# Kernel tuning notes

Hardware: AMD Instinct MI355X
Metric: run time of the kernel (lower is better)

## Reference

```python
import jax, jax.numpy as jnp
import numpy as np

DIM = 1024
HEADS = 16
HEAD_DIM = DIM // HEADS

def setup_inputs() -> dict:
    key = jax.random.key(0)
    ks = jax.random.split(key, 6)
    s = 0.02
    return {
        "x": jax.random.normal(ks[0], (2, 2048, DIM), dtype=jnp.float32),
        "w_qkv": jax.random.normal(ks[1], (DIM, 3 * DIM), dtype=jnp.float32) * s,
        "w_proj": jax.random.normal(ks[2], (DIM, DIM), dtype=jnp.float32) * s,
        "b_proj": jnp.zeros((DIM,), dtype=jnp.float32),
        "ln_gamma": jnp.ones((DIM,), dtype=jnp.float32),
        "ln_beta": jnp.zeros((DIM,), dtype=jnp.float32),
    }

def layer_norm(x, gamma, beta, eps=1e-5):
    mu = jnp.mean(x, axis=-1, keepdims=True)
    var = jnp.var(x, axis=-1, keepdims=True)
    return (x - mu) * jax.lax.rsqrt(var + eps) * gamma + beta

def reference(x, w_qkv, w_proj, b_proj, ln_gamma, ln_beta):
    B, N, C = x.shape
    residual = x
    h = layer_norm(x, ln_gamma, ln_beta)
    qkv = h @ w_qkv  # [B,N,3C]
    qkv = qkv.reshape(B, N, 3, HEADS, HEAD_DIM)
    q = jnp.transpose(qkv[:, :, 0], (0, 2, 1, 3))  # [B,H,N,D]
    k = jnp.transpose(qkv[:, :, 1], (0, 2, 1, 3))
    v = jnp.transpose(qkv[:, :, 2], (0, 2, 1, 3))
    scale = 1.0 / jnp.sqrt(jnp.float32(HEAD_DIM))
    attn = jnp.einsum('bhqd,bhkd->bhqk', q, k) * scale
    attn = jax.nn.softmax(attn, axis=-1)
    out = jnp.einsum('bhqk,bhkd->bhqd', attn, v)  # [B,H,N,D]
    out = jnp.transpose(out, (0, 2, 1, 3)).reshape(B, N, C)
    out = out @ w_proj + b_proj
    return out + residual
```

## Files before the change

kernel.cpp:

```cpp
#include <hip/hip_runtime.h>

#define DIM   1024
#define HEADS 16
#define HDIM  64
#define BATCH 2
#define SEQ   2048
#define TOK   (BATCH*SEQ)
#define MEG   1048576

typedef __bf16 bf16x8 __attribute__((ext_vector_type(8)));
typedef float  f32x4  __attribute__((ext_vector_type(4)));

__device__ __forceinline__ float b2f(ushort u) {
    union { unsigned int u32; float f; } x; x.u32 = ((unsigned int)u) << 16; return x.f;
}
__device__ __forceinline__ ushort f2b(float f) {
    union { float f; unsigned int u32; } x; x.f = f;
    unsigned int r = x.u32 + 0x7FFFu + ((x.u32 >> 16) & 1u);
    return (ushort)(r >> 16);
}
__device__ __forceinline__ unsigned int pack2bf(float a, float b) {
    union { float f; unsigned int u; } xa, xb; xa.f = a; xb.f = b;
    return (xb.u & 0xFFFF0000u) | (xa.u >> 16);
}
__device__ __forceinline__ void gload_lds16(const ushort* g, void* l) {
    __builtin_amdgcn_global_load_lds((const __attribute__((address_space(1))) void*)g,
                                     (__attribute__((address_space(3))) void*)l, 16, 0, 0);
}

__global__ void transpose_f2b_k(const float* __restrict__ src, ushort* __restrict__ dst,
                                int R, int Cc) {
    __shared__ ushort tile[32][33];
    int c0 = blockIdx.x * 32, r0 = blockIdx.y * 32;
    int tx = threadIdx.x, ty = threadIdx.y;
#pragma unroll
    for (int i = 0; i < 4; i++)
        tile[ty + 8 * i][tx] = f2b(src[(long)(r0 + ty + 8 * i) * Cc + c0 + tx]);
    __syncthreads();
#pragma unroll
    for (int i = 0; i < 4; i++)
        dst[(long)(c0 + ty + 8 * i) * R + r0 + tx] = tile[tx][ty + 8 * i];
}

__global__ __launch_bounds__(256)
void ln_k(const float* __restrict__ x, const float* __restrict__ gamma,
          const float* __restrict__ beta, ushort* __restrict__ h) {
    __shared__ float red[8];
    int row = blockIdx.x, tid = threadIdx.x;
    const float* xr = x + (long)row * DIM;
    float4 xv = *(const float4*)(xr + tid * 4);
    float s1 = xv.x + xv.y + xv.z + xv.w;
    float s2 = xv.x * xv.x + xv.y * xv.y + xv.z * xv.z + xv.w * xv.w;
#pragma unroll
    for (int off = 32; off; off >>= 1) {
        s1 += __shfl_down(s1, off);
        s2 += __shfl_down(s2, off);
    }
    int wid = tid >> 6, lane = tid & 63;
    if (lane == 0) { red[wid * 2] = s1; red[wid * 2 + 1] = s2; }
    __syncthreads();
    s1 = red[0] + red[2] + red[4] + red[6];
    s2 = red[1] + red[3] + red[5] + red[7];
    float mu  = s1 * (1.0f / DIM);
    float var = s2 * (1.0f / DIM) - mu * mu;
    float rs  = rsqrtf(var + 1e-5f);
    float4 gv = *(const float4*)(gamma + tid * 4);
    float4 bv = *(const float4*)(beta + tid * 4);
    ushort4 ov;
    ov.x = f2b((xv.x - mu) * rs * gv.x + bv.x);
    ov.y = f2b((xv.y - mu) * rs * gv.y + bv.y);
    ov.z = f2b((xv.z - mu) * rs * gv.z + bv.z);
    ov.w = f2b((xv.w - mu) * rs * gv.w + bv.w);
    *(ushort4*)(h + (long)row * DIM + tid * 4) = ov;
}

__global__ __launch_bounds__(256, 3)
void gemm_qkv_k(const ushort* __restrict__ A, const ushort* __restrict__ Bt,
                ushort* __restrict__ qp, ushort* __restrict__ kp, ushort* __restrict__ vp) {
    __shared__ ushort smem[16384];
    int tid  = threadIdx.x;
    int wid  = tid >> 6, lane = tid & 63;
    int quad = lane >> 4, l16 = lane & 15;
    int wm = wid >> 1, wn = wid & 1;
    int rowbase = blockIdx.y * 128;
    int colbase = blockIdx.x * 128;

    f32x4 acc[4][4];
#pragma unroll
    for (int i = 0; i < 4; i++)
#pragma unroll
        for (int j = 0; j < 4; j++) acc[i][j] = (f32x4){0.f, 0.f, 0.f, 0.f};

    for (int k0 = 0; k0 < DIM; k0 += 64) {
#pragma unroll
        for (int p = 0; p < 2; p++) {
            int c = wid * 2 + p;
            int r = c * 16 + (lane >> 2);
            int ac = (lane & 3) * 8;
#pragma unroll
            for (int pnl = 0; pnl < 2; pnl++) {
                int cc = k0 + pnl * 32 + ac;
                gload_lds16(A  + (long)(rowbase + r) * DIM + cc,
                            &smem[pnl * 4096 + c * 16 * 32]);
                gload_lds16(Bt + (long)(colbase + r) * DIM + cc,
                            &smem[8192 + pnl * 4096 + c * 16 * 32]);
            }
        }
        __syncthreads();
#pragma unroll
        for (int pnl = 0; pnl < 2; pnl++) {
            bf16x8 fa[4], fb[4];
#pragma unroll
            for (int t = 0; t < 4; t++)
                fa[t] = *(const bf16x8*)(&smem[pnl * 4096 + (wm * 64 + t * 16 + l16) * 32 + quad * 8]);
#pragma unroll
            for (int t = 0; t < 4; t++)
                fb[t] = *(const bf16x8*)(&smem[8192 + pnl * 4096 + (wn * 64 + t * 16 + l16) * 32 + quad * 8]);
#pragma unroll
            for (int i = 0; i < 4; i++)
#pragma unroll
                for (int j = 0; j < 4; j++)
                    acc[i][j] = __builtin_amdgcn_mfma_f32_16x16x32_bf16(fa[i], fb[j], acc[i][j], 0, 0, 0);
        }
        __syncthreads();
    }

    if (colbase >= 2048) {
#pragma unroll
        for (int i = 0; i < 4; i++)
#pragma unroll
            for (int j = 0; j < 4; j++) {
                int cl = wn * 64 + j * 16 + l16;
                int rl = wm * 64 + i * 16 + quad * 4;
#pragma unroll
                for (int r = 0; r < 4; r++)
                    smem[cl * 128 + rl + r] = f2b(acc[i][j][r]);
            }
        __syncthreads();
        int b = rowbase >> 11, nnb = rowbase & 2047;
        int hbase = (colbase - 2048) >> 6;
#pragma unroll
        for (int i = 0; i < 8; i++) {
            int id = i * 256 + tid;
            int cl = id >> 4;
            int off = (id & 15) * 8;
            int hh = hbase + (cl >> 6), d = cl & 63;
            uint4 val = *(const uint4*)(&smem[cl * 128 + off]);
            *(uint4*)(vp + (((long)b * HEADS + hh) * HDIM + d) * SEQ + nnb + off) = val;
        }
    } else {
#pragma unroll
        for (int i = 0; i < 4; i++)
#pragma unroll
            for (int j = 0; j < 4; j++) {
                int m0  = rowbase + wm * 64 + i * 16 + quad * 4;
                int col = colbase + wn * 64 + j * 16 + l16;
                int part = col >> 10, rem = col & 1023;
                int head = rem >> 6, d = rem & 63;
                ushort* dst = (part == 0) ? qp : kp;
#pragma unroll
                for (int r = 0; r < 4; r++) {
                    float v = acc[i][j][r];
                    int mm = m0 + r;
                    int b = mm >> 11, nn = mm & 2047;
                    float sv = (part == 0) ? v * 0.125f : v;
                    dst[((((long)b * HEADS + head) * SEQ + nn) << 6) + d] = f2b(sv);
                }
            }
    }
}

__global__ __launch_bounds__(256, 3)
void gemm_proj_k(const ushort* __restrict__ A, const ushort* __restrict__ Bt,
                 const float* __restrict__ bias, const float* __restrict__ xres,
                 float* __restrict__ outp) {
    __shared__ ushort As[2][128][32];
    __shared__ ushort Bs[2][64][32];
    int tid  = threadIdx.x;
    int wid  = tid >> 6, lane = tid & 63;
    int quad = lane >> 4, l16 = lane & 15;
    int rowbase = blockIdx.y * 128;
    int colbase = blockIdx.x * 64;
    int arow = lane >> 2, acol = (lane & 3) * 8;

    f32x4 acc[2][4];
#pragma unroll
    for (int i = 0; i < 2; i++)
#pragma unroll
        for (int j = 0; j < 4; j++) acc[i][j] = (f32x4){0.f, 0.f, 0.f, 0.f};

    for (int k0 = 0; k0 < DIM; k0 += 64) {
#pragma unroll
        for (int p = 0; p < 2; p++) {
            int c = wid * 2 + p;
            int r = c * 16 + arow;
            int mm = rowbase + r;
            int bq = mm >> 11, nn = mm & 2047;
#pragma unroll
            for (int pnl = 0; pnl < 2; pnl++) {
                int cc = k0 + pnl * 32 + acol;
                int head = cc >> 6, d = cc & 63;
                gload_lds16(A + ((((long)bq * HEADS + head) * SEQ + nn) << 6) + d,
                            &As[pnl][c * 16][0]);
            }
        }
        {
            int r = wid * 16 + arow;
#pragma unroll
            for (int pnl = 0; pnl < 2; pnl++) {
                int cc = k0 + pnl * 32 + acol;
                gload_lds16(Bt + (long)(colbase + r) * DIM + cc, &Bs[pnl][wid * 16][0]);
            }
        }
        __syncthreads();
#pragma unroll
        for (int pnl = 0; pnl < 2; pnl++) {
            bf16x8 fa[2], fb[4];
#pragma unroll
            for (int t = 0; t < 2; t++)
                fa[t] = *(const bf16x8*)(&As[pnl][wid * 32 + t * 16 + l16][quad * 8]);
#pragma unroll
            for (int t = 0; t < 4; t++)
                fb[t] = *(const bf16x8*)(&Bs[pnl][t * 16 + l16][quad * 8]);
#pragma unroll
            for (int i = 0; i < 2; i++)
#pragma unroll
                for (int j = 0; j < 4; j++)
                    acc[i][j] = __builtin_amdgcn_mfma_f32_16x16x32_bf16(fa[i], fb[j], acc[i][j], 0, 0, 0);
        }
        __syncthreads();
    }

#pragma unroll
    for (int i = 0; i < 2; i++)
#pragma unroll
        for (int j = 0; j < 4; j++) {
            int m0  = rowbase + wid * 32 + i * 16 + quad * 4;
            int col = colbase + j * 16 + l16;
#pragma unroll
            for (int r = 0; r < 4; r++) {
                int mm = m0 + r;
                outp[(long)mm * DIM + col] = acc[i][j][r] + bias[col] + xres[(long)mm * DIM + col];
            }
        }
}

__global__ __launch_bounds__(256, 2)
void attn_k(ushort* qio, const ushort* __restrict__ k,
            const ushort* __restrict__ vt) {
    __shared__ ushort Kp[2][2][2304];
    __shared__ ushort Vs[2][4608];
    __shared__ ushort plds[4][2][1152];
    int bh = blockIdx.y;
    int tid = threadIdx.x, wid = tid >> 6, lane = tid & 63;
    int quad = lane >> 4, l16 = lane & 15;
    ushort* qh = qio + (long)bh * SEQ * HDIM;
    const ushort* kh = k  + (long)bh * SEQ * HDIM;
    const ushort* vh = vt + (long)bh * HDIM * SEQ;

    int krow = tid & 31, kc8 = (tid >> 5) * 8;
    int kpan = kc8 >> 5, kcp = kc8 & 31;
    int koff = krow * 72 + kcp;
    int vrow = tid & 63, vcol = (tid >> 6) * 8;
    int voff = vrow * 72 + vcol;

    int qrow0 = blockIdx.x * 128 + wid * 32;
    bf16x8 qf[2][2];
#pragma unroll
    for (int s = 0; s < 2; s++) {
        qf[s][0] = *(const bf16x8*)(qh + (long)(qrow0 + s * 16 + l16) * HDIM + quad * 8);
        qf[s][1] = *(const bf16x8*)(qh + (long)(qrow0 + s * 16 + l16) * HDIM + 32 + quad * 8);
    }

    f32x4 o[2][4];
    f32x4 lac[2][2];
#pragma unroll
    for (int s = 0; s < 2; s++) {
#pragma unroll
        for (int dc = 0; dc < 4; dc++) o[s][dc] = (f32x4){0.f, 0.f, 0.f, 0.f};
        lac[s][0] = (f32x4){0.f, 0.f, 0.f, 0.f};
        lac[s][1] = (f32x4){0.f, 0.f, 0.f, 0.f};
    }

    uint4 kreg = *(const uint4*)(kh + (long)krow * HDIM + kc8);
    uint4 vreg = *(const uint4*)(vh + (long)vrow * SEQ + vcol);
    *(uint4*)(&Kp[0][kpan][koff]) = kreg;
    *(uint4*)(&Vs[0][voff]) = vreg;

    const int NIT = SEQ / 32;
    for (int it = 0; it < NIT; ++it) {
        int buf = it & 1;
        if (it + 1 < NIT) {
            int kt = (it + 1) * 32;
            kreg = *(const uint4*)(kh + (long)(kt + krow) * HDIM + kc8);
            vreg = *(const uint4*)(vh + (long)vrow * SEQ + kt + vcol);
        }
        __syncthreads();

        bf16x8 kb[2][2];
#pragma unroll
        for (int t = 0; t < 2; t++)
#pragma unroll
            for (int p = 0; p < 2; p++)
                kb[t][p] = *(const bf16x8*)(&Kp[buf][p][(t * 16 + l16) * 72 + quad * 8]);

        f32x4 sc[2][2];
#pragma unroll
        for (int s = 0; s < 2; s++)
#pragma unroll
            for (int t = 0; t < 2; t++) {
                f32x4 z = (f32x4){0.f, 0.f, 0.f, 0.f};
                z = __builtin_amdgcn_mfma_f32_16x16x32_bf16(kb[t][0], qf[s][0], z, 0, 0, 0);
                z = __builtin_amdgcn_mfma_f32_16x16x32_bf16(kb[t][1], qf[s][1], z, 0, 0, 0);
                sc[s][t] = z;
            }

#pragma unroll
        for (int s = 0; s < 2; s++)
#pragma unroll
            for (int t = 0; t < 2; t++) {
                float e0 = __expf(sc[s][t][0]);
                float e1 = __expf(sc[s][t][1]);
                float e2 = __expf(sc[s][t][2]);
                float e3 = __expf(sc[s][t][3]);
                lac[s][t] += (f32x4){e0, e1, e2, e3};
                uint2 pk;
                pk.x = pack2bf(e0, e1);
                pk.y = pack2bf(e2, e3);
                *(uint2*)(&plds[wid][s][l16 * 72 + t * 16 + quad * 4]) = pk;
            }
        asm volatile("s_waitcnt lgkmcnt(0)" ::: "memory");

        bf16x8 pf[2];
#pragma unroll
        for (int s = 0; s < 2; s++)
            pf[s] = *(const bf16x8*)(&plds[wid][s][l16 * 72 + quad * 8]);
#pragma unroll
        for (int dc = 0; dc < 4; dc++) {
            bf16x8 vfb = *(const bf16x8*)(&Vs[buf][(dc * 16 + l16) * 72 + quad * 8]);
#pragma unroll
            for (int s = 0; s < 2; s++)
                o[s][dc] = __builtin_amdgcn_mfma_f32_16x16x32_bf16(pf[s], vfb, o[s][dc], 0, 0, 0);
        }

        if (it + 1 < NIT) {
            *(uint4*)(&Kp[buf ^ 1][kpan][koff]) = kreg;
            *(uint4*)(&Vs[buf ^ 1][voff]) = vreg;
        }
    }

#pragma unroll
    for (int s = 0; s < 2; s++) {
        f32x4 lv = lac[s][0] + lac[s][1];
        float t = lv[0] + lv[1] + lv[2] + lv[3];
        t += __shfl_xor(t, 16);
        t += __shfl_xor(t, 32);
        float linv_q = 1.0f / t;
        float linv[4];
#pragma unroll
        for (int r = 0; r < 4; r++)
            linv[r] = __shfl(linv_q, quad * 4 + r);
        int rowo = qrow0 + s * 16 + quad * 4;
#pragma unroll
        for (int dc = 0; dc < 4; dc++)
#pragma unroll
            for (int r = 0; r < 4; r++)
                qh[(long)(rowo + r) * HDIM + dc * 16 + l16] = f2b(o[s][dc][r] * linv[r]);
    }
}

extern "C" void kernel_launch(void* const* d_in, const int* in_sizes, int n_in,
                              void* d_out, int out_size, void* d_ws, size_t ws_size,
                              hipStream_t stream) {
    const float* x      = (const float*)d_in[0];
    const float* w_qkv  = (const float*)d_in[1];
    const float* w_proj = (const float*)d_in[2];
    const float* b_proj = (const float*)d_in[3];
    const float* gamma  = (const float*)d_in[4];
    const float* beta   = (const float*)d_in[5];
    float* out = (float*)d_out;

    ushort* ws   = (ushort*)d_ws;
    ushort* h    = ws;
    ushort* wqt  = ws + (size_t)4 * MEG;
    ushort* qb   = ws + (size_t)7 * MEG;
    ushort* kb   = ws + (size_t)11 * MEG;
    ushort* vtb  = ws + (size_t)15 * MEG;

    transpose_f2b_k<<<dim3(3 * DIM / 32, DIM / 32), dim3(32, 8), 0, stream>>>(
        w_qkv, wqt, DIM, 3 * DIM);
    ln_k<<<dim3(TOK), dim3(256), 0, stream>>>(x, gamma, beta, h);
    gemm_qkv_k<<<dim3(3 * DIM / 128, TOK / 128), dim3(256), 0, stream>>>(
        h, wqt, qb, kb, vtb);
    attn_k<<<dim3(SEQ / 128, BATCH * HEADS), dim3(256), 0, stream>>>(qb, kb, vtb);
    transpose_f2b_k<<<dim3(DIM / 32, DIM / 32), dim3(32, 8), 0, stream>>>(
        w_proj, kb, DIM, DIM);
    gemm_proj_k<<<dim3(DIM / 64, TOK / 128), dim3(256), 0, stream>>>(
        qb, kb, b_proj, x, out);
}
```

Baseline: 193.5 us.

## Rewrite attention with 32x32 MFMA, register-only P transpose and exp2

Rewrites the attention kernel to use 32x32x16 bf16 MFMA tiles. The P matrix moves from score to PV operand layout in registers via cvt_pk_bf16 and permlane32_swap instead of a round trip through LDS. The softmax scale now folds log2(e) into the Q scaling so raw v_exp_f32 replaces __expf, and K/V LDS tiles use XOR swizzles instead of padding. This cuts LDS use enough to raise occupancy to 4 blocks per CU, and s_setprio is added around the MFMA sections. The trade-offs are higher register pressure from the larger accumulators and a dependence on gfx950-specific instructions.

```diff
diff --git a/kernel.cpp b/kernel.cpp
--- a/kernel.cpp
+++ b/kernel.cpp
@@ -10,6 +10,7 @@
 
 typedef __bf16 bf16x8 __attribute__((ext_vector_type(8)));
 typedef float  f32x4  __attribute__((ext_vector_type(4)));
+typedef float  f32x16 __attribute__((ext_vector_type(16)));
 
 __device__ __forceinline__ float b2f(ushort u) {
     union { unsigned int u32; float f; } x; x.u32 = ((unsigned int)u) << 16; return x.f;
@@ -19,13 +20,18 @@
     unsigned int r = x.u32 + 0x7FFFu + ((x.u32 >> 16) & 1u);
     return (ushort)(r >> 16);
 }
-__device__ __forceinline__ unsigned int pack2bf(float a, float b) {
-    union { float f; unsigned int u; } xa, xb; xa.f = a; xb.f = b;
-    return (xb.u & 0xFFFF0000u) | (xa.u >> 16);
-}
 __device__ __forceinline__ void gload_lds16(const ushort* g, void* l) {
     __builtin_amdgcn_global_load_lds((const __attribute__((address_space(1))) void*)g,
                                      (__attribute__((address_space(3))) void*)l, 16, 0, 0);
+}
+__device__ __forceinline__ float fexp2(float x) {
+    float r; asm("v_exp_f32 %0, %1" : "=v"(r) : "v"(x)); return r;
+}
+__device__ __forceinline__ unsigned int cvtpk_bf16(float lo, float hi) {
+    unsigned int r; asm("v_cvt_pk_bf16_f32 %0, %1, %2" : "=v"(r) : "v"(lo), "v"(hi)); return r;
+}
+__device__ __forceinline__ void plane32swap(unsigned int &a, unsigned int &b) {
+    asm("v_permlane32_swap_b32 %0, %1" : "+v"(a), "+v"(b));
 }
 
 __global__ void transpose_f2b_k(const float* __restrict__ src, ushort* __restrict__ dst,
@@ -163,7 +169,7 @@
                     float v = acc[i][j][r];
                     int mm = m0 + r;
                     int b = mm >> 11, nn = mm & 2047;
-                    float sv = (part == 0) ? v * 0.125f : v;
+                    float sv = (part == 0) ? v * 0.18033688011f : v;
                     dst[((((long)b * HEADS + head) * SEQ + nn) << 6) + d] = f2b(sv);
                 }
             }
@@ -245,127 +251,109 @@
         }
 }
 
-__global__ __launch_bounds__(256, 2)
-void attn_k(ushort* qio, const ushort* __restrict__ k,
+__global__ __launch_bounds__(256, 4)
+void attn_k(ushort* qio, const ushort* __restrict__ kg,
             const ushort* __restrict__ vt) {
-    __shared__ ushort Kp[2][2][2304];
-    __shared__ ushort Vs[2][4608];
-    __shared__ ushort plds[4][2][1152];
+    __shared__ __align__(16) ushort Kp[2][2048];
+    __shared__ __align__(16) ushort Vs[2][2048];
     int bh = blockIdx.y;
     int tid = threadIdx.x, wid = tid >> 6, lane = tid & 63;
-    int quad = lane >> 4, l16 = lane & 15;
+    int l31 = lane & 31, hi = lane >> 5;
     ushort* qh = qio + (long)bh * SEQ * HDIM;
-    const ushort* kh = k  + (long)bh * SEQ * HDIM;
+    const ushort* kh = kg + (long)bh * SEQ * HDIM;
     const ushort* vh = vt + (long)bh * HDIM * SEQ;
 
-    int krow = tid & 31, kc8 = (tid >> 5) * 8;
-    int kpan = kc8 >> 5, kcp = kc8 & 31;
-    int koff = krow * 72 + kcp;
-    int vrow = tid & 63, vcol = (tid >> 6) * 8;
-    int voff = vrow * 72 + vcol;
+    int kr = tid & 31, kc = tid >> 5;
+    int kofs = kr * 64 + ((kc ^ (kr & 7)) * 8);
+    int vrow = tid & 63;
+    int vslot = ((tid >> 6) + (vrow >> 1)) & 3;
+    int vgc = (vslot ^ (vrow & 3)) * 8;
+    int vofs = vrow * 32 + vslot * 8;
 
     int qrow0 = blockIdx.x * 128 + wid * 32;
-    bf16x8 qf[2][2];
-#pragma unroll
-    for (int s = 0; s < 2; s++) {
-        qf[s][0] = *(const bf16x8*)(qh + (long)(qrow0 + s * 16 + l16) * HDIM + quad * 8);
-        qf[s][1] = *(const bf16x8*)(qh + (long)(qrow0 + s * 16 + l16) * HDIM + 32 + quad * 8);
-    }
-
-    f32x4 o[2][4];
-    f32x4 lac[2][2];
-#pragma unroll
-    for (int s = 0; s < 2; s++) {
-#pragma unroll
-        for (int dc = 0; dc < 4; dc++) o[s][dc] = (f32x4){0.f, 0.f, 0.f, 0.f};
-        lac[s][0] = (f32x4){0.f, 0.f, 0.f, 0.f};
-        lac[s][1] = (f32x4){0.f, 0.f, 0.f, 0.f};
-    }
-
-    uint4 kreg = *(const uint4*)(kh + (long)krow * HDIM + kc8);
-    uint4 vreg = *(const uint4*)(vh + (long)vrow * SEQ + vcol);
-    *(uint4*)(&Kp[0][kpan][koff]) = kreg;
-    *(uint4*)(&Vs[0][voff]) = vreg;
+    bf16x8 qf[4];
+#pragma unroll
+    for (int ks = 0; ks < 4; ks++)
+        qf[ks] = *(const bf16x8*)(qh + (long)(qrow0 + l31) * HDIM + ks * 16 + hi * 8);
+
+    f32x16 o0 = {}, o1 = {};
+    f32x4 lac = {0.f, 0.f, 0.f, 0.f};
+
+    uint4 kreg = *(const uint4*)(kh + (long)kr * HDIM + kc * 8);
+    uint4 vreg = *(const uint4*)(vh + (long)vrow * SEQ + vgc);
+    *(uint4*)(&Kp[0][kofs]) = kreg;
+    *(uint4*)(&Vs[0][vofs]) = vreg;
 
     const int NIT = SEQ / 32;
     for (int it = 0; it < NIT; ++it) {
         int buf = it & 1;
         if (it + 1 < NIT) {
             int kt = (it + 1) * 32;
-            kreg = *(const uint4*)(kh + (long)(kt + krow) * HDIM + kc8);
-            vreg = *(const uint4*)(vh + (long)vrow * SEQ + kt + vcol);
-        }
-        __syncthreads();
-
-        bf16x8 kb[2][2];
-#pragma unroll
-        for (int t = 0; t < 2; t++)
-#pragma unroll
-            for (int p = 0; p < 2; p++)
-                kb[t][p] = *(const bf16x8*)(&Kp[buf][p][(t * 16 + l16) * 72 + quad * 8]);
-
-        f32x4 sc[2][2];
-#pragma unroll
-        for (int s = 0; s < 2; s++)
-#pragma unroll
-            for (int t = 0; t < 2; t++) {
-                f32x4 z = (f32x4){0.f, 0.f, 0.f, 0.f};
-                z = __builtin_amdgcn_mfma_f32_16x16x32_bf16(kb[t][0], qf[s][0], z, 0, 0, 0);
-                z = __builtin_amdgcn_mfma_f32_16x16x32_bf16(kb[t][1], qf[s][1], z, 0, 0, 0);
-                sc[s][t] = z;
-            }
-
-#pragma unroll
-        for (int s = 0; s < 2; s++)
-#pragma unroll
-            for (int t = 0; t < 2; t++) {
-                float e0 = __expf(sc[s][t][0]);
-                float e1 = __expf(sc[s][t][1]);
-                float e2 = __expf(sc[s][t][2]);
-                float e3 = __expf(sc[s][t][3]);
-                lac[s][t] += (f32x4){e0, e1, e2, e3};
-                uint2 pk;
-                pk.x = pack2bf(e0, e1);
-                pk.y = pack2bf(e2, e3);
-                *(uint2*)(&plds[wid][s][l16 * 72 + t * 16 + quad * 4]) = pk;
-            }
-        asm volatile("s_waitcnt lgkmcnt(0)" ::: "memory");
-
-        bf16x8 pf[2];
-#pragma unroll
-        for (int s = 0; s < 2; s++)
-            pf[s] = *(const bf16x8*)(&plds[wid][s][l16 * 72 + quad * 8]);
-#pragma unroll
-        for (int dc = 0; dc < 4; dc++) {
-            bf16x8 vfb = *(const bf16x8*)(&Vs[buf][(dc * 16 + l16) * 72 + quad * 8]);
-#pragma unroll
-            for (int s = 0; s < 2; s++)
-                o[s][dc] = __builtin_amdgcn_mfma_f32_16x16x32_bf16(pf[s], vfb, o[s][dc], 0, 0, 0);
-        }
+            kreg = *(const uint4*)(kh + (long)(kt + kr) * HDIM + kc * 8);
+            vreg = *(const uint4*)(vh + (long)vrow * SEQ + kt + vgc);
+        }
+        __syncthreads();
+
+        f32x16 sc = {};
+        __builtin_amdgcn_s_setprio(1);
+#pragma unroll
+        for (int ks = 0; ks < 4; ks++) {
+            bf16x8 kb = *(const bf16x8*)(
+                &Kp[buf][l31 * 64 + (((2 * ks + hi) ^ (l31 & 7)) * 8)]);
+            sc = __builtin_amdgcn_mfma_f32_32x32x16_bf16(kb, qf[ks], sc, 0, 0, 0);
+        }
+        __builtin_amdgcn_s_setprio(0);
+
+        float e[16];
+#pragma unroll
+        for (int r = 0; r < 16; r++) e[r] = fexp2(sc[r]);
+#pragma unroll
+        for (int r = 0; r < 4; r++)
+            lac += (f32x4){e[4 * r], e[4 * r + 1], e[4 * r + 2], e[4 * r + 3]};
+
+        unsigned int pk0 = cvtpk_bf16(e[0], e[1]),   pk1 = cvtpk_bf16(e[2], e[3]);
+        unsigned int pk2 = cvtpk_bf16(e[4], e[5]),   pk3 = cvtpk_bf16(e[6], e[7]);
+        unsigned int pk4 = cvtpk_bf16(e[8], e[9]),   pk5 = cvtpk_bf16(e[10], e[11]);
+        unsigned int pk6 = cvtpk_bf16(e[12], e[13]), pk7 = cvtpk_bf16(e[14], e[15]);
+        plane32swap(pk0, pk2);
+        plane32swap(pk1, pk3);
+        plane32swap(pk4, pk6);
+        plane32swap(pk5, pk7);
+        union { unsigned int u[4]; bf16x8 v; } pa0, pa1;
+        pa0.u[0] = pk0; pa0.u[1] = pk1; pa0.u[2] = pk2; pa0.u[3] = pk3;
+        pa1.u[0] = pk4; pa1.u[1] = pk5; pa1.u[2] = pk6; pa1.u[3] = pk7;
+
+        __builtin_amdgcn_s_setprio(1);
+        {
+            int d0 = l31;
+            bf16x8 v00 = *(const bf16x8*)(&Vs[buf][d0 * 32 + ((hi ^ (d0 & 3)) * 8)]);
+            bf16x8 v01 = *(const bf16x8*)(&Vs[buf][d0 * 32 + (((2 + hi) ^ (d0 & 3)) * 8)]);
+            o0 = __builtin_amdgcn_mfma_f32_32x32x16_bf16(pa0.v, v00, o0, 0, 0, 0);
+            o0 = __builtin_amdgcn_mfma_f32_32x32x16_bf16(pa1.v, v01, o0, 0, 0, 0);
+            int d1 = 32 + l31;
+            bf16x8 v10 = *(const bf16x8*)(&Vs[buf][d1 * 32 + ((hi ^ (d1 & 3)) * 8)]);
+            bf16x8 v11 = *(const bf16x8*)(&Vs[buf][d1 * 32 + (((2 + hi) ^ (d1 & 3)) * 8)]);
+            o1 = __builtin_amdgcn_mfma_f32_32x32x16_bf16(pa0.v, v10, o1, 0, 0, 0);
+            o1 = __builtin_amdgcn_mfma_f32_32x32x16_bf16(pa1.v, v11, o1, 0, 0, 0);
+        }
+        __builtin_amdgcn_s_setprio(0);
 
         if (it + 1 < NIT) {
-            *(uint4*)(&Kp[buf ^ 1][kpan][koff]) = kreg;
-            *(uint4*)(&Vs[buf ^ 1][voff]) = vreg;
-        }
-    }
-
-#pragma unroll
-    for (int s = 0; s < 2; s++) {
-        f32x4 lv = lac[s][0] + lac[s][1];
-        float t = lv[0] + lv[1] + lv[2] + lv[3];
-        t += __shfl_xor(t, 16);
-        t += __shfl_xor(t, 32);
-        float linv_q = 1.0f / t;
-        float linv[4];
-#pragma unroll
-        for (int r = 0; r < 4; r++)
-            linv[r] = __shfl(linv_q, quad * 4 + r);
-        int rowo = qrow0 + s * 16 + quad * 4;
-#pragma unroll
-        for (int dc = 0; dc < 4; dc++)
-#pragma unroll
-            for (int r = 0; r < 4; r++)
-                qh[(long)(rowo + r) * HDIM + dc * 16 + l16] = f2b(o[s][dc][r] * linv[r]);
+            *(uint4*)(&Kp[buf ^ 1][kofs]) = kreg;
+            *(uint4*)(&Vs[buf ^ 1][vofs]) = vreg;
+        }
+    }
+
+    float t = lac[0] + lac[1] + lac[2] + lac[3];
+    t += __shfl_xor(t, 32);
+    float linv = 1.0f / t;
+#pragma unroll
+    for (int r = 0; r < 16; r++) {
+        int qrow = (r & 3) + 8 * (r >> 2) + 4 * hi;
+        float lr = __shfl(linv, qrow);
+        long ro = (long)(qrow0 + qrow) * HDIM;
+        qh[ro + l31]      = f2b(o0[r] * lr);
+        qh[ro + 32 + l31] = f2b(o1[r] * lr);
     }
 }
 
```

Result: faster. 183.3 us (-5.3%).
